# Kernel optimization log

Hardware: AMD Instinct MI355X
Metric: run time of the kernel (lower is better)

## Reference

```python
import jax, jax.numpy as jnp
import numpy as np

N = 10000      # nodes
E = 320000     # edges (avg degree 32)
D_IN = 128
D_H = 256
D_C = 32       # comm_dim
D_OUT = 64


def setup_inputs() -> dict:
    key = jax.random.key(0)
    ks = jax.random.split(key, 14)
    p = lambda k, shape: jax.random.normal(k, shape, jnp.float32) * 0.02
    return {
        "x": jax.random.normal(ks[0], (N, D_IN), jnp.float32),
        "edge_index": jax.random.randint(ks[1], (2, E), 0, N),
        "W_in": p(ks[2], (D_IN, D_H)), "b_in": jnp.zeros((D_H,), jnp.float32),
        "Wq": p(ks[3], (D_H, D_C)),   "bq": jnp.zeros((D_C,), jnp.float32),
        "Wk": p(ks[4], (D_H, D_C)),   "bk": jnp.zeros((D_C,), jnp.float32),
        "Wv": p(ks[5], (D_H, D_H)),   "bv": jnp.zeros((D_H,), jnp.float32),
        "W1": p(ks[6], (2 * D_H, D_H)), "b1": jnp.zeros((D_H,), jnp.float32),
        "W2": p(ks[7], (D_H, D_OUT)),  "b2": jnp.zeros((D_OUT,), jnp.float32),
    }


def reference(x, edge_index, W_in, b_in, Wq, bq, Wk, bk, Wv, bv, W1, b1, W2, b2):
    n = x.shape[0]
    h = x @ W_in + b_in                       # [N, D_H]
    q = h @ Wq + bq                           # [N, D_C]
    k = h @ Wk + bk                           # [N, D_C]
    v = h @ Wv + bv                           # [N, D_H]
    scores = (q @ k.T) / np.sqrt(q.shape[-1]).astype(np.float32)  # [N, N]
    # torch: zeros -> scatter 1 at edges -> masked_fill(==0, -inf);
    # edge positions keep value 1.0 ADDED to scores (faithful quirk).
    mask = jnp.full((n, n), -jnp.inf, jnp.float32)
    mask = mask.at[edge_index[0], edge_index[1]].set(1.0)
    w = jax.nn.softmax(scores + mask, axis=-1)
    w = jnp.nan_to_num(w, nan=0.0)            # rows with no edges -> all zeros
    comm = w @ v                              # [N, D_H]
    combined = jnp.concatenate([h, comm], axis=-1)  # [N, 2*D_H]
    return jax.nn.relu(combined @ W1 + b1) @ W2 + b2  # [N, D_OUT]
```

## Files before the change

### kernel.cpp

```cpp
#include <hip/hip_runtime.h>
#include <stdint.h>
#include <stddef.h>

constexpr int N_NODES = 10000;
constexpr int N_EDGES = 320000;
constexpr int DIM_IN  = 128;
constexpr int DIM_H   = 256;
constexpr int DIM_C   = 32;
constexpr int DIM_OUT = 64;
constexpr int DIM_QKV = DIM_C + DIM_C + DIM_H;
constexpr int DIM_QK  = 2 * DIM_C;
constexpr int DIM_CAT = 2 * DIM_H;
constexpr float SCALE = 0.17677669529663687f;
constexpr int MAXD = 192;
constexpr float VSCALE = 64.0f;
constexpr int PAD = 40;
constexpr int HP  = 264;

#if __has_builtin(__builtin_amdgcn_cvt_pk_f32_fp8) && __has_builtin(__builtin_amdgcn_cvt_pk_fp8_f32)
#define V_FP8 1
#else
#define V_FP8 0
#endif

constexpr size_t alignw(size_t w) { return (w + 15) & ~size_t(15); }
constexpr size_t OFF_DEG   = 0;
constexpr size_t OFF_COL   = alignw(OFF_DEG + N_NODES);
constexpr size_t OFF_QK    = alignw(OFF_COL + (size_t)N_NODES * MAXD);
constexpr size_t OFF_BQKV  = alignw(OFF_QK + (size_t)N_NODES * DIM_QK);
constexpr size_t OFF_VT    = alignw(OFF_BQKV + DIM_QKV);
constexpr size_t OFF_CATBF = alignw(OFF_VT + (size_t)N_NODES * DIM_H / 2);
constexpr size_t OFF_WINT  = alignw(OFF_CATBF + (size_t)N_NODES * DIM_CAT / 2);
constexpr size_t OFF_WQKVT = alignw(OFF_WINT + (size_t)DIM_H * DIM_IN / 2);
constexpr size_t OFF_W1T   = alignw(OFF_WQKVT + (size_t)DIM_QKV * DIM_H / 2);
constexpr size_t OFF_W2T   = alignw(OFF_W1T + (size_t)DIM_H * DIM_CAT / 2);

typedef __attribute__((ext_vector_type(8))) short short8;
typedef __attribute__((ext_vector_type(4))) float floatx4;
typedef __attribute__((ext_vector_type(2))) float floatx2;

#define MFMA16 __builtin_amdgcn_mfma_f32_16x16x32_bf16

__device__ inline unsigned short f2bf(float f) {
    uint32_t u = __builtin_bit_cast(uint32_t, f);
    uint32_t r = (u + 0x7fffu + ((u >> 16) & 1u)) >> 16;
    return (unsigned short)r;
}
__device__ inline float bf2f_lo(uint32_t u) { return __builtin_bit_cast(float, u << 16); }
__device__ inline float bf2f_hi(uint32_t u) { return __builtin_bit_cast(float, u & 0xffff0000u); }

__global__ void prep(const int* __restrict__ ei,
                     const float* __restrict__ W_in,
                     const float* __restrict__ Wq, const float* __restrict__ Wk,
                     const float* __restrict__ Wv,
                     const float* __restrict__ bq, const float* __restrict__ bk,
                     const float* __restrict__ bv,
                     const float* __restrict__ W1, const float* __restrict__ W2,
                     int* __restrict__ deg, int* __restrict__ col,
                     unsigned short* __restrict__ WinT, unsigned short* __restrict__ WqkvT,
                     unsigned short* __restrict__ W1T, unsigned short* __restrict__ W2T,
                     float* __restrict__ bqkv)
{
    const int i0 = blockIdx.x * blockDim.x + threadIdx.x;
    const int stride = gridDim.x * blockDim.x;
    for (int e = i0; e < N_EDGES; e += stride) {
        int src = ei[e];
        int dst = ei[N_EDGES + e];
        int slot = atomicAdd(&deg[src], 1);
        if (slot < MAXD) col[src * MAXD + slot] = dst;
    }
    for (int idx = i0; idx < DIM_IN * DIM_H; idx += stride) {
        int k = idx >> 8, n = idx & 255;
        WinT[n * DIM_IN + k] = f2bf(W_in[idx]);
    }
    for (int idx = i0; idx < DIM_H * DIM_C; idx += stride) {
        int k = idx >> 5, n = idx & 31;
        WqkvT[n * DIM_H + k] = f2bf(Wq[idx]);
    }
    for (int idx = i0; idx < DIM_H * DIM_C; idx += stride) {
        int k = idx >> 5, n = idx & 31;
        WqkvT[(DIM_C + n) * DIM_H + k] = f2bf(Wk[idx]);
    }
    for (int idx = i0; idx < DIM_H * DIM_H; idx += stride) {
        int k = idx >> 8, n = idx & 255;
        WqkvT[(2 * DIM_C + n) * DIM_H + k] = f2bf(Wv[idx]);
    }
    for (int idx = i0; idx < DIM_CAT * DIM_H; idx += stride) {
        int k = idx >> 8, n = idx & 255;
        W1T[n * DIM_CAT + k] = f2bf(W1[idx]);
    }
    for (int idx = i0; idx < DIM_H * DIM_OUT; idx += stride) {
        int k = idx >> 6, n = idx & 63;
        W2T[n * DIM_H + k] = f2bf(W2[idx]);
    }
    for (int idx = i0; idx < DIM_QKV; idx += stride)
        bqkv[idx] = (idx < DIM_C) ? bq[idx]
                  : (idx < 2 * DIM_C) ? bk[idx - DIM_C] : bv[idx - 2 * DIM_C];
}

__global__ __launch_bounds__(256)
void gemm12(const float* __restrict__ x,
            const unsigned short* __restrict__ WinT, const float* __restrict__ b_in,
            const unsigned short* __restrict__ WqkvT, const float* __restrict__ bqkv,
            unsigned short* __restrict__ cat_bf, float* __restrict__ qk,
            unsigned short* __restrict__ v_tab)
{
    __shared__ short hS[64 * HP];
    __shared__ short Bs[320 * PAD];
    short* As = Bs + 256 * PAD;
    const int tid   = threadIdx.x;
    const int wave  = tid >> 6;
    const int lane  = tid & 63;
    const int quad  = lane >> 4;
    const int col16 = lane & 15;
    const int sr    = tid >> 2;
    const int sc    = (tid & 3) * 8;
    const int row0  = blockIdx.x * 64;

    floatx4 acc[16] = {};
    for (int k0 = 0; k0 < DIM_IN; k0 += 32) {
        {
            int gr = row0 + sr;
            float4 a = {}, b = {};
            if (gr < N_NODES) {
                const float4* xp = (const float4*)(x + (size_t)gr * DIM_IN + k0 + sc);
                a = xp[0]; b = xp[1];
            }
            uint4 o;
            o.x = (uint32_t)f2bf(a.x) | ((uint32_t)f2bf(a.y) << 16);
            o.y = (uint32_t)f2bf(a.z) | ((uint32_t)f2bf(a.w) << 16);
            o.z = (uint32_t)f2bf(b.x) | ((uint32_t)f2bf(b.y) << 16);
            o.w = (uint32_t)f2bf(b.z) | ((uint32_t)f2bf(b.w) << 16);
            *(uint4*)(As + sr * PAD + sc) = o;
        }
        #pragma unroll
        for (int p = 0; p < 4; ++p) {
            int r = sr + p * 64;
            *(short8*)(Bs + r * PAD + sc) = *(const short8*)(WinT + (size_t)r * DIM_IN + k0 + sc);
        }
        __syncthreads();
        short8 af = *(const short8*)(As + (wave * 16 + col16) * PAD + quad * 8);
        #pragma unroll
        for (int nf = 0; nf < 16; ++nf) {
            short8 bf = *(const short8*)(Bs + (nf * 16 + col16) * PAD + quad * 8);
            acc[nf] = MFMA16(af, bf, acc[nf], 0, 0, 0);
        }
        __syncthreads();
    }
    #pragma unroll
    for (int nf = 0; nf < 16; ++nf) {
        int gc = nf * 16 + col16;
        float bia = b_in[gc];
        #pragma unroll
        for (int r = 0; r < 4; ++r) {
            int lr = wave * 16 + quad * 4 + r;
            unsigned short hv = f2bf(acc[nf][r] + bia);
            hS[lr * HP + gc] = (short)hv;
            if (row0 + lr < N_NODES) cat_bf[(size_t)(row0 + lr) * DIM_CAT + gc] = hv;
        }
    }
    __syncthreads();

    floatx4 acc2[20] = {};
    for (int k0 = 0; k0 < DIM_H; k0 += 32) {
        #pragma unroll
        for (int p = 0; p < 5; ++p) {
            int r = sr + p * 64;
            *(short8*)(Bs + r * PAD + sc) = *(const short8*)(WqkvT + (size_t)r * DIM_H + k0 + sc);
        }
        __syncthreads();
        short8 af = *(const short8*)(hS + (wave * 16 + col16) * HP + k0 + quad * 8);
        #pragma unroll
        for (int nf = 0; nf < 20; ++nf) {
            short8 bf = *(const short8*)(Bs + (nf * 16 + col16) * PAD + quad * 8);
            acc2[nf] = MFMA16(af, bf, acc2[nf], 0, 0, 0);
        }
        __syncthreads();
    }
    #pragma unroll
    for (int nf = 0; nf < 20; ++nf) {
        int gc = nf * 16 + col16;
        float bia = bqkv[gc];
        #pragma unroll
        for (int r = 0; r < 4; ++r) {
            int gr = row0 + wave * 16 + quad * 4 + r;
            if (gr >= N_NODES) continue;
            float v = acc2[nf][r] + bia;
            if (gc < DIM_QK) {
                qk[(size_t)gr * DIM_QK + gc] = v;
            } else {
#if V_FP8
                int pk = __builtin_amdgcn_cvt_pk_fp8_f32(v * VSCALE, 0.f, 0, false);
                ((unsigned char*)v_tab)[(size_t)gr * DIM_H + (gc - DIM_QK)] =
                    (unsigned char)(pk & 0xff);
#else
                v_tab[(size_t)gr * DIM_H + (gc - DIM_QK)] = f2bf(v);
#endif
            }
        }
    }
}

__global__ __launch_bounds__(256)
void attn_row(const float* __restrict__ qk, const unsigned short* __restrict__ v_tab,
              const int* __restrict__ deg, const int* __restrict__ col,
              unsigned short* __restrict__ cat_bf) {
    __shared__ int   dstS[4][MAXD];
    __shared__ float wS[4][MAXD];
    __shared__ float qS[4][DIM_C];
    const int wave = threadIdx.x >> 6;
    const int lane = threadIdx.x & 63;
    const int row = blockIdx.x * 4 + wave;
    int d = deg[row];
    if (d > MAXD) d = MAXD;
    const int* crow = col + (size_t)row * MAXD;

    for (int p = lane; p < d; p += 64) dstS[wave][p] = crow[p];
    if (lane < DIM_C) qS[wave][lane] = qk[(size_t)row * DIM_QK + lane];
    __syncthreads();

    float mysum = 0.f;
    if (d <= 64) {
        int mydst = (lane < d) ? dstS[wave][lane] : -1;
        bool dup = false;
        for (int k2 = 0; k2 < d - 1; ++k2) {
            int other = __shfl(mydst, k2, 64);
            dup = dup || (k2 < lane && other == mydst);
        }
        float w = 0.f;
        if (lane < d && !dup) {
            const float4* kp = (const float4*)(qk + (size_t)mydst * DIM_QK + DIM_C);
            float s = 0.f;
            #pragma unroll
            for (int i = 0; i < DIM_C / 4; ++i) {
                float4 b = kp[i];
                s += qS[wave][4 * i + 0] * b.x + qS[wave][4 * i + 1] * b.y
                   + qS[wave][4 * i + 2] * b.z + qS[wave][4 * i + 3] * b.w;
            }
            w = expf(s * SCALE);
        }
        wS[wave][lane] = w;
        mysum = w;
    } else {
        for (int p = lane; p < d; p += 64) {
            int mydst = dstS[wave][p];
            bool dup = false;
            for (int j = 0; j < p; ++j) dup = dup || (dstS[wave][j] == mydst);
            float w = 0.f;
            if (!dup) {
                const float4* kp = (const float4*)(qk + (size_t)mydst * DIM_QK + DIM_C);
                float s = 0.f;
                #pragma unroll
                for (int i = 0; i < DIM_C / 4; ++i) {
                    float4 b = kp[i];
                    s += qS[wave][4 * i + 0] * b.x + qS[wave][4 * i + 1] * b.y
                       + qS[wave][4 * i + 2] * b.z + qS[wave][4 * i + 3] * b.w;
                }
                w = expf(s * SCALE);
            }
            wS[wave][p] = w;
            mysum += w;
        }
    }
    #pragma unroll
    for (int off = 32; off; off >>= 1) mysum += __shfl_down(mysum, off, 64);
    float total = __shfl(mysum, 0, 64);
#if V_FP8
    float inv = (d > 0 && total > 0.f) ? 1.0f / (total * VSCALE) : 0.f;
#else
    float inv = (d > 0 && total > 0.f) ? 1.0f / total : 0.f;
#endif
    __syncthreads();

    float4 acc = make_float4(0.f, 0.f, 0.f, 0.f);
#if V_FP8
    const uint32_t* vb = (const uint32_t*)v_tab;
#else
    const uint2* vb = (const uint2*)v_tab;
#endif
    for (int p0 = 0; p0 < d; p0 += 16) {
        int j[16]; float w[16];
        #pragma unroll
        for (int t = 0; t < 16; ++t) {
            int idx = p0 + t;
            bool in = idx < d;
            j[t] = in ? dstS[wave][idx] : 0;
            w[t] = in ? wS[wave][idx] : 0.f;
        }
#if V_FP8
        uint32_t r[16];
        #pragma unroll
        for (int t = 0; t < 16; ++t) r[t] = vb[(size_t)j[t] * 64 + lane];
        #pragma unroll
        for (int t = 0; t < 16; ++t) {
            floatx2 lo = __builtin_amdgcn_cvt_pk_f32_fp8(r[t], false);
            floatx2 hi = __builtin_amdgcn_cvt_pk_f32_fp8(r[t], true);
            acc.x += w[t] * lo.x; acc.y += w[t] * lo.y;
            acc.z += w[t] * hi.x; acc.w += w[t] * hi.y;
        }
#else
        uint2 r[16];
        #pragma unroll
        for (int t = 0; t < 16; ++t) r[t] = vb[(size_t)j[t] * 64 + lane];
        #pragma unroll
        for (int t = 0; t < 16; ++t) {
            acc.x += w[t] * bf2f_lo(r[t].x);
            acc.y += w[t] * bf2f_hi(r[t].x);
            acc.z += w[t] * bf2f_lo(r[t].y);
            acc.w += w[t] * bf2f_hi(r[t].y);
        }
#endif
    }
    acc.x *= inv; acc.y *= inv; acc.z *= inv; acc.w *= inv;
    uint2 o;
    o.x = (uint32_t)f2bf(acc.x) | ((uint32_t)f2bf(acc.y) << 16);
    o.y = (uint32_t)f2bf(acc.z) | ((uint32_t)f2bf(acc.w) << 16);
    *(uint2*)(cat_bf + (size_t)row * DIM_CAT + DIM_H + lane * 4) = o;
}

__global__ __launch_bounds__(256)
void gemm_w1w2(const unsigned short* __restrict__ cat, const unsigned short* __restrict__ W1T,
               const float* __restrict__ b1, const unsigned short* __restrict__ W2T,
               const float* __restrict__ b2, float* __restrict__ out, int M)
{
    constexpr int TP = 260;
    __shared__ short As[64 * PAD];
    __shared__ short BsTs[64 * TP];
    short* Bs = BsTs;
    short* Ts = BsTs;
    const int tid   = threadIdx.x;
    const int wave  = tid >> 6;
    const int lane  = tid & 63;
    const int quad  = lane >> 4;
    const int col16 = lane & 15;
    const int row0  = blockIdx.x * 64;

    const int sr = tid >> 2;
    const int sc = (tid & 3) * 8;

    floatx4 acc[16] = {};
    for (int k0 = 0; k0 < DIM_CAT; k0 += 32) {
        {
            int gr = row0 + sr;
            short8 v = {};
            if (gr < M) v = *(const short8*)(cat + (size_t)gr * DIM_CAT + k0 + sc);
            *(short8*)(As + sr * PAD + sc) = v;
        }
        #pragma unroll
        for (int p = 0; p < 4; ++p) {
            int r = sr + p * 64;
            *(short8*)(Bs + r * PAD + sc) = *(const short8*)(W1T + (size_t)r * DIM_CAT + k0 + sc);
        }
        __syncthreads();
        short8 a = *(const short8*)(As + (wave * 16 + col16) * PAD + quad * 8);
        #pragma unroll
        for (int nf = 0; nf < 16; ++nf) {
            short8 b = *(const short8*)(Bs + (nf * 16 + col16) * PAD + quad * 8);
            acc[nf] = MFMA16(a, b, acc[nf], 0, 0, 0);
        }
        __syncthreads();
    }

    #pragma unroll
    for (int nf = 0; nf < 16; ++nf) {
        int gc = nf * 16 + col16;
        float bia = b1[gc];
        #pragma unroll
        for (int r = 0; r < 4; ++r) {
            int lr = wave * 16 + quad * 4 + r;
            float v = fmaxf(acc[nf][r] + bia, 0.f);
            Ts[lr * TP + gc] = (short)f2bf(v);
        }
    }
    __syncthreads();

    floatx4 acc2[4] = {};
    for (int k0 = 0; k0 < DIM_H; k0 += 32) {
        short8 a = *(const short8*)(Ts + (wave * 16 + col16) * TP + k0 + quad * 8);
        #pragma unroll
        for (int nf = 0; nf < 4; ++nf) {
            int brow = nf * 16 + col16;
            short8 b = *(const short8*)(W2T + (size_t)brow * DIM_H + k0 + quad * 8);
            acc2[nf] = MFMA16(a, b, acc2[nf], 0, 0, 0);
        }
    }
    #pragma unroll
    for (int nf = 0; nf < 4; ++nf) {
        int gc = nf * 16 + col16;
        float bia = b2[gc];
        #pragma unroll
        for (int r = 0; r < 4; ++r) {
            int gr = row0 + wave * 16 + quad * 4 + r;
            if (gr < M) out[(size_t)gr * DIM_OUT + gc] = acc2[nf][r] + bia;
        }
    }
}

extern "C" void kernel_launch(void* const* d_in, const int* in_sizes, int n_in,
                              void* d_out, int out_size, void* d_ws, size_t ws_size,
                              hipStream_t stream) {
    (void)in_sizes; (void)n_in; (void)out_size; (void)ws_size;
    const float* x    = (const float*)d_in[0];
    const int*   ei   = (const int*)d_in[1];
    const float* W_in = (const float*)d_in[2];
    const float* b_in = (const float*)d_in[3];
    const float* Wq   = (const float*)d_in[4];
    const float* bq   = (const float*)d_in[5];
    const float* Wk   = (const float*)d_in[6];
    const float* bk   = (const float*)d_in[7];
    const float* Wv   = (const float*)d_in[8];
    const float* bv   = (const float*)d_in[9];
    const float* W1   = (const float*)d_in[10];
    const float* b1   = (const float*)d_in[11];
    const float* W2   = (const float*)d_in[12];
    const float* b2   = (const float*)d_in[13];
    float* out = (float*)d_out;

    uint32_t* ws      = (uint32_t*)d_ws;
    int*      deg     = (int*)(ws + OFF_DEG);
    int*      col     = (int*)(ws + OFF_COL);
    float*    qk      = (float*)(ws + OFF_QK);
    float*    bqkv    = (float*)(ws + OFF_BQKV);
    unsigned short* v_tab  = (unsigned short*)(ws + OFF_VT);
    unsigned short* cat_bf = (unsigned short*)(ws + OFF_CATBF);
    unsigned short* WinT   = (unsigned short*)(ws + OFF_WINT);
    unsigned short* WqkvT  = (unsigned short*)(ws + OFF_WQKVT);
    unsigned short* W1T    = (unsigned short*)(ws + OFF_W1T);
    unsigned short* W2T    = (unsigned short*)(ws + OFF_W2T);

    hipMemsetAsync(deg, 0, N_NODES * sizeof(int), stream);
    prep<<<640, 256, 0, stream>>>(ei, W_in, Wq, Wk, Wv, bq, bk, bv, W1, W2,
                                  deg, col, WinT, WqkvT, W1T, W2T, bqkv);
    gemm12<<<(N_NODES + 63) / 64, 256, 0, stream>>>(
        x, WinT, b_in, WqkvT, bqkv, cat_bf, qk, v_tab);
    attn_row<<<N_NODES / 4, 256, 0, stream>>>(qk, v_tab, deg, col, cat_bf);
    gemm_w1w2<<<(N_NODES + 63) / 64, 256, 0, stream>>>(
        cat_bf, W1T, b1, W2T, b2, out, N_NODES);
}
```

Baseline: 189.3 us.

## Halve GEMM row tiles to 32 and split output columns across waves

Both dense GEMM kernels (the input and QKV projection, and the W1/W2 MLP) now process 32 rows per block instead of 64, which roughly doubles the grid so more CUs are busy. Each wave now computes a 2x4 (or 2x5) MFMA tile over its own slice of output columns instead of its own 16 rows across all columns. That reuses A fragments within a wave and lowers per-wave accumulator registers. The cost is that each block loads the full weight tiles for half as many rows, so total weight traffic through LDS doubles.

```diff
diff --git a/kernel.cpp b/kernel.cpp
--- a/kernel.cpp
+++ b/kernel.cpp
@@ -105,9 +105,9 @@
             unsigned short* __restrict__ cat_bf, float* __restrict__ qk,
             unsigned short* __restrict__ v_tab)
 {
-    __shared__ short hS[64 * HP];
+    __shared__ short hS[32 * HP];
+    __shared__ short As[32 * PAD];
     __shared__ short Bs[320 * PAD];
-    short* As = Bs + 256 * PAD;
     const int tid   = threadIdx.x;
     const int wave  = tid >> 6;
     const int lane  = tid & 63;
@@ -115,23 +115,20 @@
     const int col16 = lane & 15;
     const int sr    = tid >> 2;
     const int sc    = (tid & 3) * 8;
-    const int row0  = blockIdx.x * 64;
-
-    floatx4 acc[16] = {};
+    const int ar    = tid >> 3;
+    const int ac    = (tid & 7) * 4;
+    const int row0  = blockIdx.x * 32;
+
+    floatx4 acc[2][4] = {};
     for (int k0 = 0; k0 < DIM_IN; k0 += 32) {
         {
-            int gr = row0 + sr;
-            float4 a = {}, b = {};
-            if (gr < N_NODES) {
-                const float4* xp = (const float4*)(x + (size_t)gr * DIM_IN + k0 + sc);
-                a = xp[0]; b = xp[1];
-            }
-            uint4 o;
+            int gr = row0 + ar;
+            float4 a = {};
+            if (gr < N_NODES) a = *(const float4*)(x + (size_t)gr * DIM_IN + k0 + ac);
+            uint2 o;
             o.x = (uint32_t)f2bf(a.x) | ((uint32_t)f2bf(a.y) << 16);
             o.y = (uint32_t)f2bf(a.z) | ((uint32_t)f2bf(a.w) << 16);
-            o.z = (uint32_t)f2bf(b.x) | ((uint32_t)f2bf(b.y) << 16);
-            o.w = (uint32_t)f2bf(b.z) | ((uint32_t)f2bf(b.w) << 16);
-            *(uint4*)(As + sr * PAD + sc) = o;
+            *(uint2*)(As + ar * PAD + ac) = o;
         }
         #pragma unroll
         for (int p = 0; p < 4; ++p) {
@@ -139,29 +136,37 @@
             *(short8*)(Bs + r * PAD + sc) = *(const short8*)(WinT + (size_t)r * DIM_IN + k0 + sc);
         }
         __syncthreads();
-        short8 af = *(const short8*)(As + (wave * 16 + col16) * PAD + quad * 8);
-        #pragma unroll
-        for (int nf = 0; nf < 16; ++nf) {
-            short8 bf = *(const short8*)(Bs + (nf * 16 + col16) * PAD + quad * 8);
-            acc[nf] = MFMA16(af, bf, acc[nf], 0, 0, 0);
-        }
+        short8 af[2], bfr[4];
+        #pragma unroll
+        for (int m = 0; m < 2; ++m)
+            af[m] = *(const short8*)(As + (m * 16 + col16) * PAD + quad * 8);
+        #pragma unroll
+        for (int n = 0; n < 4; ++n)
+            bfr[n] = *(const short8*)(Bs + (wave * 64 + n * 16 + col16) * PAD + quad * 8);
+        #pragma unroll
+        for (int m = 0; m < 2; ++m)
+            #pragma unroll
+            for (int n = 0; n < 4; ++n)
+                acc[m][n] = MFMA16(af[m], bfr[n], acc[m][n], 0, 0, 0);
         __syncthreads();
     }
     #pragma unroll
-    for (int nf = 0; nf < 16; ++nf) {
-        int gc = nf * 16 + col16;
-        float bia = b_in[gc];
-        #pragma unroll
-        for (int r = 0; r < 4; ++r) {
-            int lr = wave * 16 + quad * 4 + r;
-            unsigned short hv = f2bf(acc[nf][r] + bia);
-            hS[lr * HP + gc] = (short)hv;
-            if (row0 + lr < N_NODES) cat_bf[(size_t)(row0 + lr) * DIM_CAT + gc] = hv;
-        }
-    }
+    for (int m = 0; m < 2; ++m)
+        #pragma unroll
+        for (int n = 0; n < 4; ++n) {
+            int gc = wave * 64 + n * 16 + col16;
+            float bia = b_in[gc];
+            #pragma unroll
+            for (int r = 0; r < 4; ++r) {
+                int lr = m * 16 + quad * 4 + r;
+                unsigned short hv = f2bf(acc[m][n][r] + bia);
+                hS[lr * HP + gc] = (short)hv;
+                if (row0 + lr < N_NODES) cat_bf[(size_t)(row0 + lr) * DIM_CAT + gc] = hv;
+            }
+        }
     __syncthreads();
 
-    floatx4 acc2[20] = {};
+    floatx4 acc2[2][5] = {};
     for (int k0 = 0; k0 < DIM_H; k0 += 32) {
         #pragma unroll
         for (int p = 0; p < 5; ++p) {
@@ -169,36 +174,44 @@
             *(short8*)(Bs + r * PAD + sc) = *(const short8*)(WqkvT + (size_t)r * DIM_H + k0 + sc);
         }
         __syncthreads();
-        short8 af = *(const short8*)(hS + (wave * 16 + col16) * HP + k0 + quad * 8);
-        #pragma unroll
-        for (int nf = 0; nf < 20; ++nf) {
-            short8 bf = *(const short8*)(Bs + (nf * 16 + col16) * PAD + quad * 8);
-            acc2[nf] = MFMA16(af, bf, acc2[nf], 0, 0, 0);
-        }
+        short8 af[2], bfr[5];
+        #pragma unroll
+        for (int m = 0; m < 2; ++m)
+            af[m] = *(const short8*)(hS + (m * 16 + col16) * HP + k0 + quad * 8);
+        #pragma unroll
+        for (int n = 0; n < 5; ++n)
+            bfr[n] = *(const short8*)(Bs + (wave * 80 + n * 16 + col16) * PAD + quad * 8);
+        #pragma unroll
+        for (int m = 0; m < 2; ++m)
+            #pragma unroll
+            for (int n = 0; n < 5; ++n)
+                acc2[m][n] = MFMA16(af[m], bfr[n], acc2[m][n], 0, 0, 0);
         __syncthreads();
     }
     #pragma unroll
-    for (int nf = 0; nf < 20; ++nf) {
-        int gc = nf * 16 + col16;
-        float bia = bqkv[gc];
-        #pragma unroll
-        for (int r = 0; r < 4; ++r) {
-            int gr = row0 + wave * 16 + quad * 4 + r;
-            if (gr >= N_NODES) continue;
-            float v = acc2[nf][r] + bia;
-            if (gc < DIM_QK) {
-                qk[(size_t)gr * DIM_QK + gc] = v;
-            } else {
+    for (int m = 0; m < 2; ++m)
+        #pragma unroll
+        for (int n = 0; n < 5; ++n) {
+            int gc = wave * 80 + n * 16 + col16;
+            float bia = bqkv[gc];
+            #pragma unroll
+            for (int r = 0; r < 4; ++r) {
+                int gr = row0 + m * 16 + quad * 4 + r;
+                if (gr >= N_NODES) continue;
+                float v = acc2[m][n][r] + bia;
+                if (gc < DIM_QK) {
+                    qk[(size_t)gr * DIM_QK + gc] = v;
+                } else {
 #if V_FP8
-                int pk = __builtin_amdgcn_cvt_pk_fp8_f32(v * VSCALE, 0.f, 0, false);
-                ((unsigned char*)v_tab)[(size_t)gr * DIM_H + (gc - DIM_QK)] =
-                    (unsigned char)(pk & 0xff);
+                    int pk = __builtin_amdgcn_cvt_pk_fp8_f32(v * VSCALE, 0.f, 0, false);
+                    ((unsigned char*)v_tab)[(size_t)gr * DIM_H + (gc - DIM_QK)] =
+                        (unsigned char)(pk & 0xff);
 #else
-                v_tab[(size_t)gr * DIM_H + (gc - DIM_QK)] = f2bf(v);
+                    v_tab[(size_t)gr * DIM_H + (gc - DIM_QK)] = f2bf(v);
 #endif
+                }
             }
         }
-    }
 }
 
 __global__ __launch_bounds__(256)
@@ -324,8 +337,8 @@
                const float* __restrict__ b2, float* __restrict__ out, int M)
 {
     constexpr int TP = 260;
-    __shared__ short As[64 * PAD];
-    __shared__ short BsTs[64 * TP];
+    __shared__ short As[32 * PAD];
+    __shared__ short BsTs[256 * PAD];
     short* Bs = BsTs;
     short* Ts = BsTs;
     const int tid   = threadIdx.x;
@@ -333,14 +346,14 @@
     const int lane  = tid & 63;
     const int quad  = lane >> 4;
     const int col16 = lane & 15;
-    const int row0  = blockIdx.x * 64;
+    const int row0  = blockIdx.x * 32;
 
     const int sr = tid >> 2;
     const int sc = (tid & 3) * 8;
 
-    floatx4 acc[16] = {};
+    floatx4 acc[2][4] = {};
     for (int k0 = 0; k0 < DIM_CAT; k0 += 32) {
-        {
+        if (sr < 32) {
             int gr = row0 + sr;
             short8 v = {};
             if (gr < M) v = *(const short8*)(cat + (size_t)gr * DIM_CAT + k0 + sc);
@@ -352,46 +365,52 @@
             *(short8*)(Bs + r * PAD + sc) = *(const short8*)(W1T + (size_t)r * DIM_CAT + k0 + sc);
         }
         __syncthreads();
-        short8 a = *(const short8*)(As + (wave * 16 + col16) * PAD + quad * 8);
-        #pragma unroll
-        for (int nf = 0; nf < 16; ++nf) {
-            short8 b = *(const short8*)(Bs + (nf * 16 + col16) * PAD + quad * 8);
-            acc[nf] = MFMA16(a, b, acc[nf], 0, 0, 0);
-        }
+        short8 af[2], bfr[4];
+        #pragma unroll
+        for (int m = 0; m < 2; ++m)
+            af[m] = *(const short8*)(As + (m * 16 + col16) * PAD + quad * 8);
+        #pragma unroll
+        for (int n = 0; n < 4; ++n)
+            bfr[n] = *(const short8*)(Bs + (wave * 64 + n * 16 + col16) * PAD + quad * 8);
+        #pragma unroll
+        for (int m = 0; m < 2; ++m)
+            #pragma unroll
+            for (int n = 0; n < 4; ++n)
+                acc[m][n] = MFMA16(af[m], bfr[n], acc[m][n], 0, 0, 0);
         __syncthreads();
     }
 
     #pragma unroll
-    for (int nf = 0; nf < 16; ++nf) {
-        int gc = nf * 16 + col16;
-        float bia = b1[gc];
+    for (int m = 0; m < 2; ++m)
+        #pragma unroll
+        for (int n = 0; n < 4; ++n) {
+            int gc = wave * 64 + n * 16 + col16;
+            float bia = b1[gc];
+            #pragma unroll
+            for (int r = 0; r < 4; ++r) {
+                int lr = m * 16 + quad * 4 + r;
+                Ts[lr * TP + gc] = (short)f2bf(fmaxf(acc[m][n][r] + bia, 0.f));
+            }
+        }
+    __syncthreads();
+
+    floatx4 acc2[2] = {};
+    for (int k0 = 0; k0 < DIM_H; k0 += 32) {
+        short8 b = *(const short8*)(W2T + (size_t)(wave * 16 + col16) * DIM_H + k0 + quad * 8);
+        #pragma unroll
+        for (int m = 0; m < 2; ++m) {
+            short8 a = *(const short8*)(Ts + (m * 16 + col16) * TP + k0 + quad * 8);
+            acc2[m] = MFMA16(a, b, acc2[m], 0, 0, 0);
+        }
+    }
+    #pragma unroll
+    for (int m = 0; m < 2; ++m) {
+        int gc = wave * 16 + col16;
+        float bia = b2[gc];
         #pragma unroll
         for (int r = 0; r < 4; ++r) {
-            int lr = wave * 16 + quad * 4 + r;
-            float v = fmaxf(acc[nf][r] + bia, 0.f);
-            Ts[lr * TP + gc] = (short)f2bf(v);
-        }
-    }
-    __syncthreads();
-
-    floatx4 acc2[4] = {};
-    for (int k0 = 0; k0 < DIM_H; k0 += 32) {
-        short8 a = *(const short8*)(Ts + (wave * 16 + col16) * TP + k0 + quad * 8);
-        #pragma unroll
-        for (int nf = 0; nf < 4; ++nf) {
-            int brow = nf * 16 + col16;
-            short8 b = *(const short8*)(W2T + (size_t)brow * DIM_H + k0 + quad * 8);
-            acc2[nf] = MFMA16(a, b, acc2[nf], 0, 0, 0);
-        }
-    }
-    #pragma unroll
-    for (int nf = 0; nf < 4; ++nf) {
-        int gc = nf * 16 + col16;
-        float bia = b2[gc];
-        #pragma unroll
-        for (int r = 0; r < 4; ++r) {
-            int gr = row0 + wave * 16 + quad * 4 + r;
-            if (gr < M) out[(size_t)gr * DIM_OUT + gc] = acc2[nf][r] + bia;
+            int gr = row0 + m * 16 + quad * 4 + r;
+            if (gr < M) out[(size_t)gr * DIM_OUT + gc] = acc2[m][r] + bia;
         }
     }
 }
@@ -431,9 +450,9 @@
     hipMemsetAsync(deg, 0, N_NODES * sizeof(int), stream);
     prep<<<640, 256, 0, stream>>>(ei, W_in, Wq, Wk, Wv, bq, bk, bv, W1, W2,
                                   deg, col, WinT, WqkvT, W1T, W2T, bqkv);
-    gemm12<<<(N_NODES + 63) / 64, 256, 0, stream>>>(
+    gemm12<<<(N_NODES + 31) / 32, 256, 0, stream>>>(
         x, WinT, b_in, WqkvT, bqkv, cat_bf, qk, v_tab);
     attn_row<<<N_NODES / 4, 256, 0, stream>>>(qk, v_tab, deg, col, cat_bf);
-    gemm_w1w2<<<(N_NODES + 63) / 64, 256, 0, stream>>>(
+    gemm_w1w2<<<(N_NODES + 31) / 32, 256, 0, stream>>>(
         cat_bf, W1T, b1, W2T, b2, out, N_NODES);
 }
```

Measured after the change: 168.8 us. 1.12x faster.
